# Optimization experiments

Measured on AMD Instinct MI355X. Metric: run time of the kernel, lower is better.

The kernel has to match this reference:

```python
import jax, jax.numpy as jnp
import numpy as np

B, NQ, NV, DIM, HEADS, K = 2, 2048, 2048, 256, 8, 8
HD = DIM // HEADS
HID = 4 * DIM
SCALE = HD ** -0.5
EPS = 1e-5


def setup_inputs() -> dict:
    key = jax.random.key(0)
    ks = jax.random.split(key, 40)
    r = lambda i, s: jax.random.normal(ks[i], s, jnp.float32) * 0.02
    inp = {
        'q': jax.random.normal(ks[0], (B, NQ, DIM), jnp.float32),
        'v': jax.random.normal(ks[1], (B, NV, DIM), jnp.float32),
        'q_pos': jax.random.normal(ks[2], (B, NQ, 3), jnp.float32),
        'v_pos': jax.random.normal(ks[3], (B, NV, 3), jnp.float32),
        'self_knn_index': jax.random.randint(ks[4], (B, NQ, K), 0, NQ, jnp.int32),
        'cross_knn_index': jax.random.randint(ks[5], (B, NQ, K), 0, NV, jnp.int32),
        # LayerNorms (gamma=1, beta=0)
        'norm1_g': jnp.ones(DIM), 'norm1_b': jnp.zeros(DIM),
        'normq_g': jnp.ones(DIM), 'normq_b': jnp.zeros(DIM),
        'normv_g': jnp.ones(DIM), 'normv_b': jnp.zeros(DIM),
        'norm2_g': jnp.ones(DIM), 'norm2_b': jnp.zeros(DIM),
        # self-attention (qkv_bias=False), proj has bias
        'sa_qkv_w': r(6, (DIM, 3 * DIM)),
        'sa_proj_w': r(7, (DIM, DIM)), 'sa_proj_b': jnp.zeros(DIM),
        # cross-attention: q proj and kv proj (no bias), out proj with bias
        'ca_q_w': r(8, (DIM, DIM)),
        'ca_kv_w': r(9, (DIM, 2 * DIM)),
        'ca_proj_w': r(10, (DIM, DIM)), 'ca_proj_b': jnp.zeros(DIM),
        # MLP
        'fc1_w': r(11, (DIM, HID)), 'fc1_b': jnp.zeros(HID),
        'fc2_w': r(12, (HID, DIM)), 'fc2_b': jnp.zeros(DIM),
        # kNN maps
        'knn_w': r(13, (2 * DIM, DIM)), 'knn_b': jnp.zeros(DIM),
        'merge_w': r(14, (2 * DIM, DIM)), 'merge_b': jnp.zeros(DIM),
        'knnx_w': r(15, (2 * DIM, DIM)), 'knnx_b': jnp.zeros(DIM),
        'mergex_w': r(16, (2 * DIM, DIM)), 'mergex_b': jnp.zeros(DIM),
    }
    return inp


def _ln(x, g, b):
    m = x.mean(-1, keepdims=True)
    var = x.var(-1, keepdims=True)
    return (x - m) / jnp.sqrt(var + EPS) * g + b


def _heads(x):  # [B,N,DIM] -> [B,H,N,HD]
    Bx, N, _ = x.shape
    return x.reshape(Bx, N, HEADS, HD).transpose(0, 2, 1, 3)


def _attend(qh, kh, vh, proj_w, proj_b):
    a = jax.nn.softmax(jnp.einsum('bhqd,bhkd->bhqk', qh, kh) * SCALE, axis=-1)
    o = jnp.einsum('bhqk,bhkd->bhqd', a, vh)
    Bx, _, N, _ = o.shape
    o = o.transpose(0, 2, 1, 3).reshape(Bx, N, DIM)
    return o @ proj_w + proj_b


_gather = jax.vmap(lambda pts, idx: pts[idx])  # ([N,D],[Nq,K]) -> [Nq,K,D]


def _knn_feature(qn, vn, idx):  # gather -> diff/cat -> [B,Nq,K,2D]
    local = _gather(vn, idx)                      # [B,Nq,K,D]
    qe = qn[:, :, None, :]                        # [B,Nq,1,D]
    return jnp.concatenate([local - qe, jnp.broadcast_to(qe, local.shape)], -1)


def reference(q, v, q_pos, v_pos, self_knn_index, cross_knn_index,
              norm1_g, norm1_b, normq_g, normq_b, normv_g, normv_b,
              norm2_g, norm2_b, sa_qkv_w, sa_proj_w, sa_proj_b,
              ca_q_w, ca_kv_w, ca_proj_w, ca_proj_b,
              fc1_w, fc1_b, fc2_w, fc2_b,
              knn_w, knn_b, merge_w, merge_b,
              knnx_w, knnx_b, mergex_w, mergex_b):
    # ---- self-attention block with self-kNN branch ----
    nq = _ln(q, norm1_g, norm1_b)
    qkv = nq @ sa_qkv_w
    qh, kh, vh = (_heads(t) for t in jnp.split(qkv, 3, axis=-1))
    sa_out = _attend(qh, kh, vh, sa_proj_w, sa_proj_b)
    f = _knn_feature(nq, nq, self_knn_index)
    knn_out = jax.nn.leaky_relu(f @ knn_w + knn_b, 0.2).max(axis=-2)
    q1 = jnp.concatenate([sa_out, knn_out], -1) @ merge_w + merge_b
    q = q + q1
    # ---- cross-attention block with cross-kNN branch ----
    nq2 = _ln(q, normq_g, normq_b)
    nv = _ln(v, normv_g, normv_b)
    qh = _heads(nq2 @ ca_q_w)
    kh, vh = (_heads(t) for t in jnp.split(nv @ ca_kv_w, 2, axis=-1))
    ca_out = _attend(qh, kh, vh, ca_proj_w, ca_proj_b)
    f = _knn_feature(nq2, nv, cross_knn_index)
    knnx_out = jax.nn.leaky_relu(f @ knnx_w + knnx_b, 0.2).max(axis=-2)
    q2 = jnp.concatenate([ca_out, knnx_out], -1) @ mergex_w + mergex_b
    q = q + q2
    # ---- MLP block ----
    h = _ln(q, norm2_g, norm2_b)
    h = jax.nn.gelu(h @ fc1_w + fc1_b, approximate=False)
    q = q + (h @ fc2_w + fc2_b)
    return q
```

## Files before the change

### kernel.cpp

```cpp
#include <hip/hip_runtime.h>
#include <math.h>

#define NQC   2048
#define NKVC  2048
#define DIMC  256
#define SCALEF 0.2550348810731232f

typedef short bfrag __attribute__((ext_vector_type(8)));
typedef float ffrag __attribute__((ext_vector_type(4)));
typedef unsigned short us8 __attribute__((ext_vector_type(8)));

__device__ __forceinline__ float gelu_exact(float x) {
    return 0.5f * x * (1.0f + erff(x * 0.70710678118654752f));
}
__device__ __forceinline__ unsigned short f2bf(float f) {
    union { float f; unsigned u; } v; v.f = f;
    unsigned r = v.u + 0x7FFFu + ((v.u >> 16) & 1u);
    return (unsigned short)(r >> 16);
}
__device__ __forceinline__ float bf2f(unsigned short u) {
    union { unsigned u; float f; } v; v.u = ((unsigned)u) << 16;
    return v.f;
}
__device__ __forceinline__ float fexp2(float x) {
    float r; asm("v_exp_f32 %0, %1" : "=v"(r) : "v"(x)); return r;
}
__device__ __forceinline__ unsigned cvt_pk_bf16(float lo, float hi) {
    unsigned r; asm("v_cvt_pk_bf16_f32 %0, %1, %2" : "=v"(r) : "v"(lo), "v"(hi));
    return r;
}

__device__ __forceinline__ void ln_row(
    const float* __restrict__ x, const float* __restrict__ g,
    const float* __restrict__ b, unsigned short* __restrict__ y, int row)
{
    int lane = threadIdx.x & 63;
    const float* xr = x + (size_t)row * DIMC + lane * 4;
    float4 vv = *(const float4*)xr;
    float s  = vv.x + vv.y + vv.z + vv.w;
    float sq = vv.x*vv.x + vv.y*vv.y + vv.z*vv.z + vv.w*vv.w;
    #pragma unroll
    for (int off = 32; off >= 1; off >>= 1) {
        s  += __shfl_xor(s, off);
        sq += __shfl_xor(sq, off);
    }
    float mean = s * (1.0f/DIMC);
    float inv  = rsqrtf(sq * (1.0f/DIMC) - mean*mean + 1e-5f);
    float4 gg = *(const float4*)(g + lane*4);
    float4 bb = *(const float4*)(b + lane*4);
    ushort4 o;
    o.x = f2bf((vv.x - mean) * inv * gg.x + bb.x);
    o.y = f2bf((vv.y - mean) * inv * gg.y + bb.y);
    o.z = f2bf((vv.z - mean) * inv * gg.z + bb.z);
    o.w = f2bf((vv.w - mean) * inv * gg.w + bb.w);
    *(ushort4*)(y + (size_t)row * DIMC + lane * 4) = o;
}

__global__ __launch_bounds__(256) void prep_ln(
    const float* __restrict__ qkv, const float* __restrict__ knn,
    const float* __restrict__ proj, const float* __restrict__ merge,
    const float* __restrict__ caq, const float* __restrict__ knnx,
    const float* __restrict__ cakv, const float* __restrict__ projx,
    const float* __restrict__ mergex, const float* __restrict__ fc1,
    const float* __restrict__ fc2, unsigned short* __restrict__ dst,
    const float* __restrict__ lx, const float* __restrict__ lg,
    const float* __restrict__ lb, unsigned short* __restrict__ ly,
    const float* __restrict__ vx, const float* __restrict__ vg,
    const float* __restrict__ vb, unsigned short* __restrict__ vy,
    const float* __restrict__ pb1, const float* __restrict__ mb1, float* __restrict__ bf1o,
    const float* __restrict__ pbx, const float* __restrict__ mbx, float* __restrict__ bfxo)
{
    if (blockIdx.x >= 3584) {
        const float* bp = (blockIdx.x == 3584) ? pb1 : pbx;
        const float* Wm = (blockIdx.x == 3584) ? merge : mergex;
        const float* bm = (blockIdx.x == 3584) ? mb1 : mbx;
        float* o        = (blockIdx.x == 3584) ? bf1o : bfxo;
        int m = threadIdx.x;
        float acc = bm[m];
        for (int k = 0; k < 256; ++k) acc += bp[k] * Wm[(size_t)k * 256 + m];
        o[m] = acc;
        return;
    }
    if (blockIdx.x >= 2560) {
        int row = (blockIdx.x - 2560) * 4 + (threadIdx.x >> 6);
        ln_row(vx, vg, vb, vy, row);
        return;
    }
    if (blockIdx.x >= 1536) {
        int row = (blockIdx.x - 1536) * 4 + (threadIdx.x >> 6);
        ln_row(lx, lg, lb, ly, row);
        return;
    }
    int e = (blockIdx.x * 256 + threadIdx.x) * 4;
    float v[4];
    float scale = 1.0f;
    if (e < 327680) {
        int n = e >> 8, k = e & 255;
        if (n < 768) {
            const float* s = qkv + (size_t)k * 768 + n;
            #pragma unroll
            for (int i = 0; i < 4; ++i) v[i] = s[(size_t)i * 768];
            if (n < 256) scale = SCALEF;
        } else if (n < 1024) {
            const float* s = knn + (size_t)k * 256 + (n - 768);
            #pragma unroll
            for (int i = 0; i < 4; ++i) v[i] = s[(size_t)i * 256];
        } else {
            const float* s = knn + (size_t)k * 256 + (n - 1024);
            #pragma unroll
            for (int i = 0; i < 4; ++i) v[i] = s[65536 + (size_t)i * 256] - s[(size_t)i * 256];
        }
    } else if (e < 393216) {
        int l = e - 327680;
        const float* s = proj + l;
        #pragma unroll
        for (int i = 0; i < 4; ++i) v[i] = s[i];
    } else if (e < 524288) {
        int l = e - 393216, n = l >> 9, k = l & 511;
        const float* s = merge + (size_t)k * 256 + n;
        #pragma unroll
        for (int i = 0; i < 4; ++i) v[i] = s[(size_t)i * 256];
    } else if (e < 655360) {
        int l = e - 524288, n = l >> 8, k = l & 255;
        if (n < 256) {
            const float* s = caq + (size_t)k * 256 + n;
            #pragma unroll
            for (int i = 0; i < 4; ++i) v[i] = s[(size_t)i * 256];
            scale = SCALEF;
        } else {
            const float* s = knnx + (size_t)k * 256 + (n - 256);
            #pragma unroll
            for (int i = 0; i < 4; ++i) v[i] = s[65536 + (size_t)i * 256] - s[(size_t)i * 256];
        }
    } else if (e < 851968) {
        int l = e - 655360, n = l >> 8, k = l & 255;
        if (n < 512) {
            const float* s = cakv + (size_t)k * 512 + n;
            #pragma unroll
            for (int i = 0; i < 4; ++i) v[i] = s[(size_t)i * 512];
        } else {
            const float* s = knnx + (size_t)k * 256 + (n - 512);
            #pragma unroll
            for (int i = 0; i < 4; ++i) v[i] = s[(size_t)i * 256];
        }
    } else if (e < 917504) {
        int l = e - 851968;
        const float* s = projx + l;
        #pragma unroll
        for (int i = 0; i < 4; ++i) v[i] = s[i];
    } else if (e < 1048576) {
        int l = e - 917504, n = l >> 9, k = l & 511;
        const float* s = mergex + (size_t)k * 256 + n;
        #pragma unroll
        for (int i = 0; i < 4; ++i) v[i] = s[(size_t)i * 256];
    } else if (e < 1310720) {
        int l = e - 1048576, n = l >> 8, k = l & 255;
        const float* s = fc1 + (size_t)k * 1024 + n;
        #pragma unroll
        for (int i = 0; i < 4; ++i) v[i] = s[(size_t)i * 1024];
    } else {
        int l = e - 1310720, n = l >> 10, k = l & 1023;
        const float* s = fc2 + (size_t)k * 256 + n;
        #pragma unroll
        for (int i = 0; i < 4; ++i) v[i] = s[(size_t)i * 256];
    }
    ushort4 o;
    o.x = f2bf(v[0] * scale); o.y = f2bf(v[1] * scale);
    o.z = f2bf(v[2] * scale); o.w = f2bf(v[3] * scale);
    *(ushort4*)(dst + e) = o;
}

__global__ __launch_bounds__(256) void ln_b(
    const float* __restrict__ x, const float* __restrict__ g,
    const float* __restrict__ b, unsigned short* __restrict__ y)
{
    ln_row(x, g, b, y, blockIdx.x * 4 + (threadIdx.x >> 6));
}

template<int ACT, int RESID, int OUTBF, int VTM>
__device__ __forceinline__ void gemm_body(
    const unsigned short* __restrict__ A, int lda,
    const unsigned short* __restrict__ Wt,
    const float* __restrict__ bias,
    const float* __restrict__ resid, int ldr,
    void* __restrict__ Cp, int ldc, int Kc, int row0, int col0,
    unsigned short (* __restrict__ Alds)[72],
    unsigned short (* __restrict__ Wlds)[72],
    unsigned short* __restrict__ vt, int vlo)
{
    const int tid = threadIdx.x;
    const int wid = tid >> 6, lane = tid & 63;
    const int lm = lane & 15, quad = lane >> 4;
    const int wr = wid >> 1, wc = wid & 1;
    const int ar = tid >> 2, ac = (tid & 3) * 16;
    const unsigned short* Ag = A  + (size_t)(row0 + ar) * lda + ac;
    const unsigned short* Wg = Wt + (size_t)(col0 + ar) * Kc  + ac;

    us8 a0 = *(const us8*)Ag;
    us8 a1 = *(const us8*)(Ag + 8);
    us8 w0 = *(const us8*)Wg;
    us8 w1 = *(const us8*)(Wg + 8);

    ffrag acc[2][2];
    #pragma unroll
    for (int mi = 0; mi < 2; ++mi)
        #pragma unroll
        for (int ni = 0; ni < 2; ++ni)
            acc[mi][ni] = (ffrag){0.f, 0.f, 0.f, 0.f};

    for (int k0 = 0;;) {
        __syncthreads();
        *(us8*)&Alds[ar][ac]   = a0;
        *(us8*)&Alds[ar][ac+8] = a1;
        *(us8*)&Wlds[ar][ac]   = w0;
        *(us8*)&Wlds[ar][ac+8] = w1;
        __syncthreads();
        k0 += 64;
        if (k0 < Kc) {
            a0 = *(const us8*)(Ag + k0);
            a1 = *(const us8*)(Ag + k0 + 8);
            w0 = *(const us8*)(Wg + k0);
            w1 = *(const us8*)(Wg + k0 + 8);
        }
        #pragma unroll
        for (int kc = 0; kc < 2; ++kc) {
            bfrag af[2], bw[2];
            #pragma unroll
            for (int mi = 0; mi < 2; ++mi)
                af[mi] = *(const bfrag*)&Alds[wr*32 + mi*16 + lm][kc*32 + quad*8];
            #pragma unroll
            for (int ni = 0; ni < 2; ++ni)
                bw[ni] = *(const bfrag*)&Wlds[wc*32 + ni*16 + lm][kc*32 + quad*8];
            #pragma unroll
            for (int mi = 0; mi < 2; ++mi)
                #pragma unroll
                for (int ni = 0; ni < 2; ++ni)
                    acc[mi][ni] = __builtin_amdgcn_mfma_f32_16x16x32_bf16(
                        af[mi], bw[ni], acc[mi][ni], 0, 0, 0);
        }
        if (k0 >= Kc) break;
    }
    if (VTM && col0 >= vlo && col0 - vlo < 256) {
        __syncthreads();
        #pragma unroll
        for (int mi = 0; mi < 2; ++mi) {
            #pragma unroll
            for (int ni = 0; ni < 2; ++ni) {
                int lr = wr*32 + mi*16 + quad*4;
                int lc = wc*32 + ni*16 + lm;
                #pragma unroll
                for (int r = 0; r < 4; ++r) {
                    int k = lr + r;
                    Alds[lc][((k & 15) << 2) | (k >> 4)] = f2bf(acc[mi][ni][r]);
                }
            }
        }
        __syncthreads();
        int d = tid >> 2, p0 = (tid & 3) * 16;
        int cv = col0 - vlo + d, hh = cv >> 5, dd = cv & 31;
        int bq = row0 >> 11, kblk = (row0 & 2047) >> 6;
        unsigned short* vp = vt + (((size_t)(bq * 8 + hh) * 32 + dd) * 2048)
                                + kblk * 64 + p0;
        *(us8*)vp       = *(const us8*)&Alds[d][p0];
        *(us8*)(vp + 8) = *(const us8*)&Alds[d][p0 + 8];
        return;
    }
    #pragma unroll
    for (int mi = 0; mi < 2; ++mi) {
        #pragma unroll
        for (int ni = 0; ni < 2; ++ni) {
            int gr = row0 + wr*32 + mi*16 + quad*4;
            int gc = col0 + wc*32 + ni*16 + lm;
            float bv = bias ? bias[gc] : 0.f;
            #pragma unroll
            for (int r = 0; r < 4; ++r) {
                float o = acc[mi][ni][r] + bv;
                if (ACT == 1) o = gelu_exact(o);
                if (RESID) o += resid[(size_t)(gr + r) * ldr + gc];
                if (OUTBF) ((unsigned short*)Cp)[(size_t)(gr + r) * ldc + gc] = f2bf(o);
                else       ((float*)Cp)[(size_t)(gr + r) * ldc + gc] = o;
            }
        }
    }
}

template<int ACT, int RESID, int OUTBF>
__global__ __launch_bounds__(256) void gemm64(
    const unsigned short* __restrict__ A, int lda,
    const unsigned short* __restrict__ Wt,
    const float* __restrict__ bias,
    const float* __restrict__ resid, int ldr,
    void* __restrict__ Cp, int ldc, int Kc)
{
    __shared__ unsigned short Alds[64][72];
    __shared__ unsigned short Wlds[64][72];
    gemm_body<ACT,RESID,OUTBF,0>(A, lda, Wt, bias, resid, ldr, Cp, ldc, Kc,
                                 blockIdx.y * 64, blockIdx.x * 64, Alds, Wlds,
                                 nullptr, 0);
}

__global__ __launch_bounds__(256) void gemm_qkv_fold(
    const unsigned short* __restrict__ XB, const unsigned short* __restrict__ WT1,
    unsigned short* __restrict__ A1,
    const unsigned short* __restrict__ WTmerge, const unsigned short* __restrict__ projbf,
    unsigned short* __restrict__ WTf1,
    const unsigned short* __restrict__ WTmergex, const unsigned short* __restrict__ projxbf,
    unsigned short* __restrict__ WTfx,
    unsigned short* __restrict__ VT)
{
    __shared__ unsigned short Alds[64][72];
    __shared__ unsigned short Wlds[64][72];
    const unsigned short *A, *Wt; unsigned short* C;
    int lda, ldc, row0, col0, vlo;
    if (blockIdx.y >= 64) {
        if (blockIdx.x >= 16) return;
        row0 = (blockIdx.x >> 2) * 64; col0 = (blockIdx.x & 3) * 64;
        lda = 512; ldc = 256; vlo = 1 << 30;
        if (blockIdx.y == 64) { A = WTmerge;  Wt = projbf;  C = WTf1; }
        else                  { A = WTmergex; Wt = projxbf; C = WTfx; }
    } else {
        A = XB; Wt = WT1; C = A1; lda = 256; ldc = 1280; vlo = 512;
        row0 = blockIdx.y * 64; col0 = blockIdx.x * 64;
    }
    gemm_body<0,0,1,1>(A, lda, Wt, nullptr, nullptr, 0, C, ldc, 256, row0, col0,
                       Alds, Wlds, VT, vlo);
}

template<int ACT, int RESID, int OUTBF>
__global__ __launch_bounds__(512) void gemm64x8(
    const unsigned short* __restrict__ A, int lda,
    const unsigned short* __restrict__ Wt,
    const float* __restrict__ bias,
    const float* __restrict__ resid, int ldr,
    void* __restrict__ Cp, int ldc, int Kc)
{
    __shared__ unsigned short Alds[2][64][72];
    __shared__ unsigned short Wlds[2][64][72];
    __shared__ float Red[64][68];
    const int tid = threadIdx.x;
    const int g = tid >> 8;
    const int t = tid & 255;
    const int wid2 = (tid >> 6) & 3, lane = tid & 63;
    const int lm = lane & 15, quad = lane >> 4;
    const int wr = wid2 >> 1, wc = wid2 & 1;
    const int row0 = blockIdx.y * 64, col0 = blockIdx.x * 64;
    const int ar = t >> 2, ac = (t & 3) * 16;
    const int KH = Kc >> 1;
    const unsigned short* Ag = A  + (size_t)(row0 + ar) * lda + g * KH + ac;
    const unsigned short* Wg = Wt + (size_t)(col0 + ar) * Kc  + g * KH + ac;

    us8 a0 = *(const us8*)Ag;
    us8 a1 = *(const us8*)(Ag + 8);
    us8 w0 = *(const us8*)Wg;
    us8 w1 = *(const us8*)(Wg + 8);

    ffrag acc[2][2];
    #pragma unroll
    for (int mi = 0; mi < 2; ++mi)
        #pragma unroll
        for (int ni = 0; ni < 2; ++ni)
            acc[mi][ni] = (ffrag){0.f, 0.f, 0.f, 0.f};

    for (int k0 = 0;;) {
        __syncthreads();
        *(us8*)&Alds[g][ar][ac]   = a0;
        *(us8*)&Alds[g][ar][ac+8] = a1;
        *(us8*)&Wlds[g][ar][ac]   = w0;
        *(us8*)&Wlds[g][ar][ac+8] = w1;
        __syncthreads();
        k0 += 64;
        if (k0 < KH) {
            a0 = *(const us8*)(Ag + k0);
            a1 = *(const us8*)(Ag + k0 + 8);
            w0 = *(const us8*)(Wg + k0);
            w1 = *(const us8*)(Wg + k0 + 8);
        }
        #pragma unroll
        for (int kc = 0; kc < 2; ++kc) {
            bfrag af[2], bw[2];
            #pragma unroll
            for (int mi = 0; mi < 2; ++mi)
                af[mi] = *(const bfrag*)&Alds[g][wr*32 + mi*16 + lm][kc*32 + quad*8];
            #pragma unroll
            for (int ni = 0; ni < 2; ++ni)
                bw[ni] = *(const bfrag*)&Wlds[g][wc*32 + ni*16 + lm][kc*32 + quad*8];
            #pragma unroll
            for (int mi = 0; mi < 2; ++mi)
                #pragma unroll
                for (int ni = 0; ni < 2; ++ni)
                    acc[mi][ni] = __builtin_amdgcn_mfma_f32_16x16x32_bf16(
                        af[mi], bw[ni], acc[mi][ni], 0, 0, 0);
        }
        if (k0 >= KH) break;
    }
    __syncthreads();
    if (g == 1) {
        #pragma unroll
        for (int mi = 0; mi < 2; ++mi)
            #pragma unroll
            for (int ni = 0; ni < 2; ++ni) {
                int lr = wr*32 + mi*16 + quad*4;
                int lc = wc*32 + ni*16 + lm;
                #pragma unroll
                for (int r = 0; r < 4; ++r)
                    Red[lr + r][lc] = acc[mi][ni][r];
            }
    }
    __syncthreads();
    if (g == 0) {
        #pragma unroll
        for (int mi = 0; mi < 2; ++mi) {
            #pragma unroll
            for (int ni = 0; ni < 2; ++ni) {
                int lr = wr*32 + mi*16 + quad*4;
                int lc = wc*32 + ni*16 + lm;
                int gr = row0 + lr;
                int gc = col0 + lc;
                float bv = bias ? bias[gc] : 0.f;
                #pragma unroll
                for (int r = 0; r < 4; ++r) {
                    float o = acc[mi][ni][r] + Red[lr + r][lc] + bv;
                    if (ACT == 1) o = gelu_exact(o);
                    if (RESID) o += resid[(size_t)(gr + r) * ldr + gc];
                    if (OUTBF) ((unsigned short*)Cp)[(size_t)(gr + r) * ldc + gc] = f2bf(o);
                    else       ((float*)Cp)[(size_t)(gr + r) * ldc + gc] = o;
                }
            }
        }
    }
}

__global__ __launch_bounds__(512) void gemm64x8f(
    const unsigned short* __restrict__ O,
    const unsigned short* __restrict__ Akn,
    const unsigned short* __restrict__ W0,
    const unsigned short* __restrict__ W1,
    const float* __restrict__ bias,
    const float* __restrict__ resid,
    float* __restrict__ Cp)
{
    __shared__ unsigned short Alds[2][64][72];
    __shared__ unsigned short Wlds[2][64][72];
    __shared__ float Red[64][68];
    const int tid = threadIdx.x;
    const int g = tid >> 8;
    const int t = tid & 255;
    const int wid2 = (tid >> 6) & 3, lane = tid & 63;
    const int lm = lane & 15, quad = lane >> 4;
    const int wr = wid2 >> 1, wc = wid2 & 1;
    const int row0 = blockIdx.y * 64, col0 = blockIdx.x * 64;
    const int ar = t >> 2, ac = (t & 3) * 16;
    const int grow = row0 + ar;

    const unsigned short* Ag = g ? Akn + (size_t)grow * 512 + ac
                                 : O   + (size_t)grow * 256 + ac;
    const unsigned short* Wg = g ? W1 + (size_t)(col0 + ar) * 512 + ac
                                 : W0 + (size_t)(col0 + ar) * 256 + ac;

    us8 a0 = *(const us8*)Ag;
    us8 a1 = *(const us8*)(Ag + 8);
    us8 w0 = *(const us8*)Wg;
    us8 w1 = *(const us8*)(Wg + 8);

    ffrag acc[2][2];
    #pragma unroll
    for (int mi = 0; mi < 2; ++mi)
        #pragma unroll
        for (int ni = 0; ni < 2; ++ni)
            acc[mi][ni] = (ffrag){0.f, 0.f, 0.f, 0.f};

    for (int k0 = 0;;) {
        __syncthreads();
        *(us8*)&Alds[g][ar][ac]   = a0;
        *(us8*)&Alds[g][ar][ac+8] = a1;
        *(us8*)&Wlds[g][ar][ac]   = w0;
        *(us8*)&Wlds[g][ar][ac+8] = w1;
        __syncthreads();
        k0 += 64;
        if (k0 < 256) {
            a0 = *(const us8*)(Ag + k0);
            a1 = *(const us8*)(Ag + k0 + 8);
            w0 = *(const us8*)(Wg + k0);
            w1 = *(const us8*)(Wg + k0 + 8);
        }
        #pragma unroll
        for (int kc = 0; kc < 2; ++kc) {
            bfrag af[2], bw[2];
            #pragma unroll
            for (int mi = 0; mi < 2; ++mi)
                af[mi] = *(const bfrag*)&Alds[g][wr*32 + mi*16 + lm][kc*32 + quad*8];
            #pragma unroll
            for (int ni = 0; ni < 2; ++ni)
                bw[ni] = *(const bfrag*)&Wlds[g][wc*32 + ni*16 + lm][kc*32 + quad*8];
            #pragma unroll
            for (int mi = 0; mi < 2; ++mi)
                #pragma unroll
                for (int ni = 0; ni < 2; ++ni)
                    acc[mi][ni] = __builtin_amdgcn_mfma_f32_16x16x32_bf16(
                        af[mi], bw[ni], acc[mi][ni], 0, 0, 0);
        }
        if (k0 >= 256) break;
    }
    __syncthreads();
    if (g == 1) {
        #pragma unroll
        for (int mi = 0; mi < 2; ++mi)
            #pragma unroll
            for (int ni = 0; ni < 2; ++ni) {
                int lr = wr*32 + mi*16 + quad*4;
                int lc = wc*32 + ni*16 + lm;
                #pragma unroll
                for (int r = 0; r < 4; ++r)
                    Red[lr + r][lc] = acc[mi][ni][r];
            }
    }
    __syncthreads();
    if (g == 0) {
        #pragma unroll
        for (int mi = 0; mi < 2; ++mi) {
            #pragma unroll
            for (int ni = 0; ni < 2; ++ni) {
                int lr = wr*32 + mi*16 + quad*4;
                int lc = wc*32 + ni*16 + lm;
                int gr = row0 + lr;
                int gc = col0 + lc;
                float bv = bias[gc];
                #pragma unroll
                for (int r = 0; r < 4; ++r)
                    Cp[(size_t)(gr + r) * 256 + gc] =
                        acc[mi][ni][r] + Red[lr + r][lc] + bv
                        + resid[(size_t)(gr + r) * 256 + gc];
            }
        }
    }
}

__global__ __launch_bounds__(256) void gemm64_dual(
    const unsigned short* __restrict__ XB,
    const unsigned short* __restrict__ NVB,
    const unsigned short* __restrict__ WT2,
    const unsigned short* __restrict__ WT3,
    unsigned short* __restrict__ A2,
    unsigned short* __restrict__ A3,
    unsigned short* __restrict__ VT)
{
    __shared__ unsigned short Alds[64][72];
    __shared__ unsigned short Wlds[64][72];
    const unsigned short* A; const unsigned short* Wt;
    unsigned short* C; int ldc, col0, vlo;
    if (blockIdx.x < 8) { A = XB;  Wt = WT2; C = A2; ldc = 512; col0 = blockIdx.x * 64; vlo = 1 << 30; }
    else                { A = NVB; Wt = WT3; C = A3; ldc = 768; col0 = (blockIdx.x - 8) * 64; vlo = 256; }
    gemm_body<0,0,1,1>(A, 256, Wt, nullptr, nullptr, 0, C, ldc, 256,
                       blockIdx.y * 64, col0, Alds, Wlds, VT, vlo);
}

__global__ __launch_bounds__(256) void attn_gather(
    const unsigned short* __restrict__ Qp, int ldq,
    const unsigned short* __restrict__ Kp, int ldk,
    const unsigned short* __restrict__ VT,
    unsigned short* __restrict__ Op,
    const unsigned short* __restrict__ P, int ldp,
    const unsigned short* __restrict__ Base, int ldb,
    const float* __restrict__ gbias, const int* __restrict__ idx,
    unsigned short* __restrict__ gout, int ldgo)
{
    __shared__ unsigned short Klds[64][40];
    __shared__ __align__(16) unsigned short Vt[32][72];
    __shared__ __align__(16) unsigned short Plds[4][16][72];
    int tid = threadIdx.x, wid = tid >> 6, lane = tid & 63;

    if (blockIdx.z >= 1) {
        int gbid = blockIdx.x + 64 * (blockIdx.y + 8 * (blockIdx.z - 1));
        int q = gbid * 4 + wid;
        int b = q >> 11;
        int c = lane * 4;
        ushort4 bu = *(const ushort4*)(Base + (size_t)q * ldb + c);
        float4 bi = *(const float4*)(gbias + c);
        float bsx = bf2f(bu.x) + bi.x, bsy = bf2f(bu.y) + bi.y;
        float bsz = bf2f(bu.z) + bi.z, bsw = bf2f(bu.w) + bi.w;
        float4 acc = make_float4(-3e38f, -3e38f, -3e38f, -3e38f);
        const int* ip = idx + (size_t)q * 8;
        #pragma unroll
        for (int k = 0; k < 8; ++k) {
            int j = ip[k];
            ushort4 pu = *(const ushort4*)(P + ((size_t)(b * NKVC + j)) * ldp + c);
            float t;
            t = bsx + bf2f(pu.x); t = t > 0.f ? t : 0.2f * t; acc.x = fmaxf(acc.x, t);
            t = bsy + bf2f(pu.y); t = t > 0.f ? t : 0.2f * t; acc.y = fmaxf(acc.y, t);
            t = bsz + bf2f(pu.z); t = t > 0.f ? t : 0.2f * t; acc.z = fmaxf(acc.z, t);
            t = bsw + bf2f(pu.w); t = t > 0.f ? t : 0.2f * t; acc.w = fmaxf(acc.w, t);
        }
        ushort4 o;
        o.x = f2bf(acc.x); o.y = f2bf(acc.y); o.z = f2bf(acc.z); o.w = f2bf(acc.w);
        *(ushort4*)(gout + (size_t)q * ldgo + c) = o;
        return;
    }

    int bb = blockIdx.x >> 5, qc = blockIdx.x & 31;
    int h = blockIdx.y;
    int hoff = h * 32;
    int lm = lane & 15, quad = lane >> 4;
    size_t qbase  = (size_t)bb * NQC;
    size_t kvbase = (size_t)bb * NKVC;
    int q0 = qc * 64 + wid * 16;

    bfrag aq = *(const bfrag*)(Qp + (qbase + q0 + lm) * (size_t)ldq + hoff + quad * 8);

    float l_r[4] = {0.f, 0.f, 0.f, 0.f};
    ffrag oacc[2];
    oacc[0] = (ffrag){0.f, 0.f, 0.f, 0.f};
    oacc[1] = (ffrag){0.f, 0.f, 0.f, 0.f};

    const int kkey = tid >> 2, kd0 = (tid & 3) * 8;
    const int vrow = tid >> 3, vp0 = (tid & 7) * 8;
    const unsigned short* kg0 = Kp + (kvbase + kkey) * (size_t)ldk + hoff + kd0;
    const unsigned short* vg0 = VT + (((size_t)bb * 8 + h) * 32 + vrow) * 2048 + vp0;

    for (int kt = 0; kt < 32; ++kt) {
        us8 kv = *(const us8*)(kg0 + (size_t)kt * 64 * ldk);
        us8 vv = *(const us8*)(vg0 + kt * 64);
        __syncthreads();
        *(us8*)&Klds[kkey][kd0] = kv;
        *(us8*)&Vt[vrow][vp0]   = vv;
        __syncthreads();

        ffrag sacc[4];
        #pragma unroll
        for (int t = 0; t < 4; ++t) {
            bfrag bk = *(const bfrag*)&Klds[t*16 + lm][quad * 8];
            sacc[t] = __builtin_amdgcn_mfma_f32_16x16x32_bf16(
                aq, bk, (ffrag){0.f,0.f,0.f,0.f}, 0, 0, 0);
        }

        #pragma unroll
        for (int r = 0; r < 4; ++r) {
            float p0 = fexp2(sacc[0][r]), p1 = fexp2(sacc[1][r]);
            float p2 = fexp2(sacc[2][r]), p3 = fexp2(sacc[3][r]);
            l_r[r] += (p0 + p1) + (p2 + p3);
            *(uint2*)&Plds[wid][quad*4 + r][lm << 2] =
                make_uint2(cvt_pk_bf16(p0, p1), cvt_pk_bf16(p2, p3));
        }
        asm volatile("s_waitcnt lgkmcnt(0)" ::: "memory");

        #pragma unroll
        for (int kc = 0; kc < 2; ++kc) {
            bfrag ap  = *(const bfrag*)&Plds[wid][lm][kc*32 + quad*8];
            bfrag bv0 = *(const bfrag*)&Vt[lm][kc*32 + quad*8];
            bfrag bv1 = *(const bfrag*)&Vt[16 + lm][kc*32 + quad*8];
            oacc[0] = __builtin_amdgcn_mfma_f32_16x16x32_bf16(ap, bv0, oacc[0], 0, 0, 0);
            oacc[1] = __builtin_amdgcn_mfma_f32_16x16x32_bf16(ap, bv1, oacc[1], 0, 0, 0);
        }
    }
    #pragma unroll
    for (int r = 0; r < 4; ++r) {
        float a = l_r[r];
        a += __shfl_xor(a, 1); a += __shfl_xor(a, 2);
        a += __shfl_xor(a, 4); a += __shfl_xor(a, 8);
        l_r[r] = 1.0f / a;
    }
    #pragma unroll
    for (int nt = 0; nt < 2; ++nt)
        #pragma unroll
        for (int r = 0; r < 4; ++r)
            Op[(qbase + q0 + quad*4 + r) * 256 + hoff + nt*16 + lm]
                = f2bf(oacc[nt][r] * l_r[r]);
}

extern "C" void kernel_launch(void* const* d_in, const int* in_sizes, int n_in,
                              void* d_out, int out_size, void* d_ws, size_t ws_size,
                              hipStream_t stream) {
    const float* q_in   = (const float*)d_in[0];
    const float* v_in   = (const float*)d_in[1];
    const int*   idx_s  = (const int*)d_in[4];
    const int*   idx_x  = (const int*)d_in[5];
    const float* n1g = (const float*)d_in[6],  *n1b = (const float*)d_in[7];
    const float* nqg = (const float*)d_in[8],  *nqb = (const float*)d_in[9];
    const float* nvg = (const float*)d_in[10], *nvb = (const float*)d_in[11];
    const float* n2g = (const float*)d_in[12], *n2b = (const float*)d_in[13];
    const float* sa_qkv_w  = (const float*)d_in[14];
    const float* sa_proj_w = (const float*)d_in[15];
    const float* sa_proj_b = (const float*)d_in[16];
    const float* ca_q_w    = (const float*)d_in[17];
    const float* ca_kv_w   = (const float*)d_in[18];
    const float* ca_proj_w = (const float*)d_in[19];
    const float* ca_proj_b = (const float*)d_in[20];
    const float* fc1_w = (const float*)d_in[21], *fc1_b = (const float*)d_in[22];
    const float* fc2_w = (const float*)d_in[23], *fc2_b = (const float*)d_in[24];
    const float* knn_w   = (const float*)d_in[25], *knn_b   = (const float*)d_in[26];
    const float* merge_w = (const float*)d_in[27], *merge_b = (const float*)d_in[28];
    const float* knnx_w  = (const float*)d_in[29], *knnx_b  = (const float*)d_in[30];
    const float* mergex_w = (const float*)d_in[31], *mergex_b = (const float*)d_in[32];
    float* out = (float*)d_out;

    unsigned short* A1      = (unsigned short*)d_ws;
    unsigned short* A2      = A1;
    unsigned short* A3      = A1 + (size_t)4096 * 512;
    unsigned short* Hb      = A1;
    unsigned short* KN      = A1 + (size_t)4096 * 1280;
    unsigned short* CC      = KN;
    unsigned short* XB      = CC + (size_t)4096 * 512;
    unsigned short* NVB     = XB + (size_t)4096 * 256;
    unsigned short* WT      = NVB + (size_t)4096 * 256;
    unsigned short* WT1     = WT;
    unsigned short* projbf  = WT + 327680;
    unsigned short* WTmerge = WT + 393216;
    unsigned short* WT2     = WT + 524288;
    unsigned short* WT3     = WT + 655360;
    unsigned short* projxbf = WT + 851968;
    unsigned short* WTmergex= WT + 917504;
    unsigned short* WTfc1   = WT + 1048576;
    unsigned short* WTfc2   = WT + 1310720;
    unsigned short* Opart   = WT + 1572864;
    unsigned short* WTf1    = Opart + (size_t)4096 * 256;
    unsigned short* WTfx    = WTf1 + 65536;
    float* bf1 = (float*)(WTfx + 65536);
    float* bfx = bf1 + 256;
    unsigned short* VT = (unsigned short*)(bfx + 256);

    dim3 blk(256), blk8(512);
    dim3 gAG(64, 8, 3);

    prep_ln<<<dim3(3586), blk, 0, stream>>>(sa_qkv_w, knn_w, sa_proj_w, merge_w,
        ca_q_w, knnx_w, ca_kv_w, ca_proj_w, mergex_w, fc1_w, fc2_w, WT,
        q_in, n1g, n1b, XB,
        v_in, nvg, nvb, NVB,
        sa_proj_b, merge_b, bf1,
        ca_proj_b, mergex_b, bfx);

    gemm_qkv_fold<<<dim3(20,66), blk, 0, stream>>>(XB, WT1, A1,
        WTmerge, projbf, WTf1, WTmergex, projxbf, WTfx, VT);
    attn_gather<<<gAG, blk, 0, stream>>>(A1, 1280, A1+256, 1280, VT,
        Opart, A1+768, 1280, A1+1024, 1280, knn_b, idx_s, CC+256, 512);
    gemm64x8f<<<dim3(4,64), blk8, 0, stream>>>(Opart, CC+256,
        WTf1, WTmerge+256, bf1, q_in, out);

    ln_b<<<dim3(1024), blk, 0, stream>>>(out, nqg, nqb, XB);
    gemm64_dual<<<dim3(20,64), blk, 0, stream>>>(XB, NVB, WT2, WT3, A2, A3, VT);
    attn_gather<<<gAG, blk, 0, stream>>>(A2, 512, A3, 768, VT,
        Opart, A3+512, 768, A2+256, 512, knnx_b, idx_x, CC+256, 512);
    gemm64x8f<<<dim3(4,64), blk8, 0, stream>>>(Opart, CC+256,
        WTfx, WTmergex+256, bfx, out, out);

    ln_b<<<dim3(1024), blk, 0, stream>>>(out, n2g, n2b, XB);
    gemm64<1,0,1><<<dim3(16,64), blk, 0, stream>>>(XB, 256, WTfc1,
        fc1_b, nullptr, 0, Hb, 1024, 256);
    gemm64x8<0,1,0><<<dim3(4,64), blk8, 0, stream>>>(Hb, 1024, WTfc2,
        fc2_b, out, 256, out, 256, 1024);
}
```

Baseline: 248.3 us.

## Fuse LayerNorm into GEMM A-tile loads and tile weight transposes via LDS

Drops the separate LayerNorm kernels (ln_b launches and the norm1 part of prep). Each GEMM block now computes row mean and variance from fp32 activations and normalizes to bf16 while loading its A tiles. This removes two launches and the bf16 round trip through global memory. In exchange, every column block recomputes the row statistics and rereads fp32 rows. The weight prep kernel also now transposes 64x64 tiles through shared memory with vectorized coalesced loads and stores, replacing strided scalar reads.

```diff
diff --git a/kernel.cpp b/kernel.cpp
--- a/kernel.cpp
+++ b/kernel.cpp
@@ -56,130 +56,149 @@
     *(ushort4*)(y + (size_t)row * DIMC + lane * 4) = o;
 }
 
-__global__ __launch_bounds__(256) void prep_ln(
+__device__ __forceinline__ void ln_frag(
+    const float* __restrict__ xr, const float* __restrict__ lng,
+    const float* __restrict__ lnb, int cc, float mean, float inv,
+    us8& o0, us8& o1)
+{
+    float4 x0 = *(const float4*)(xr + cc);
+    float4 x1 = *(const float4*)(xr + cc + 4);
+    float4 x2 = *(const float4*)(xr + cc + 8);
+    float4 x3 = *(const float4*)(xr + cc + 12);
+    float4 g0 = *(const float4*)(lng + cc);
+    float4 g1 = *(const float4*)(lng + cc + 4);
+    float4 g2 = *(const float4*)(lng + cc + 8);
+    float4 g3 = *(const float4*)(lng + cc + 12);
+    float4 b0 = *(const float4*)(lnb + cc);
+    float4 b1 = *(const float4*)(lnb + cc + 4);
+    float4 b2 = *(const float4*)(lnb + cc + 8);
+    float4 b3 = *(const float4*)(lnb + cc + 12);
+    union { us8 v; unsigned short s[8]; } u0, u1;
+    u0.s[0] = f2bf(((x0.x - mean) * inv) * g0.x + b0.x);
+    u0.s[1] = f2bf(((x0.y - mean) * inv) * g0.y + b0.y);
+    u0.s[2] = f2bf(((x0.z - mean) * inv) * g0.z + b0.z);
+    u0.s[3] = f2bf(((x0.w - mean) * inv) * g0.w + b0.w);
+    u0.s[4] = f2bf(((x1.x - mean) * inv) * g1.x + b1.x);
+    u0.s[5] = f2bf(((x1.y - mean) * inv) * g1.y + b1.y);
+    u0.s[6] = f2bf(((x1.z - mean) * inv) * g1.z + b1.z);
+    u0.s[7] = f2bf(((x1.w - mean) * inv) * g1.w + b1.w);
+    u1.s[0] = f2bf(((x2.x - mean) * inv) * g2.x + b2.x);
+    u1.s[1] = f2bf(((x2.y - mean) * inv) * g2.y + b2.y);
+    u1.s[2] = f2bf(((x2.z - mean) * inv) * g2.z + b2.z);
+    u1.s[3] = f2bf(((x2.w - mean) * inv) * g2.w + b2.w);
+    u1.s[4] = f2bf(((x3.x - mean) * inv) * g3.x + b3.x);
+    u1.s[5] = f2bf(((x3.y - mean) * inv) * g3.y + b3.y);
+    u1.s[6] = f2bf(((x3.z - mean) * inv) * g3.z + b3.z);
+    u1.s[7] = f2bf(((x3.w - mean) * inv) * g3.w + b3.w);
+    o0 = u0.v; o1 = u1.v;
+}
+
+__global__ __launch_bounds__(256) void prep_w(
     const float* __restrict__ qkv, const float* __restrict__ knn,
     const float* __restrict__ proj, const float* __restrict__ merge,
     const float* __restrict__ caq, const float* __restrict__ knnx,
     const float* __restrict__ cakv, const float* __restrict__ projx,
     const float* __restrict__ mergex, const float* __restrict__ fc1,
     const float* __restrict__ fc2, unsigned short* __restrict__ dst,
-    const float* __restrict__ lx, const float* __restrict__ lg,
-    const float* __restrict__ lb, unsigned short* __restrict__ ly,
     const float* __restrict__ vx, const float* __restrict__ vg,
     const float* __restrict__ vb, unsigned short* __restrict__ vy,
     const float* __restrict__ pb1, const float* __restrict__ mb1, float* __restrict__ bf1o,
     const float* __restrict__ pbx, const float* __restrict__ mbx, float* __restrict__ bfxo)
 {
-    if (blockIdx.x >= 3584) {
-        const float* bp = (blockIdx.x == 3584) ? pb1 : pbx;
-        const float* Wm = (blockIdx.x == 3584) ? merge : mergex;
-        const float* bm = (blockIdx.x == 3584) ? mb1 : mbx;
-        float* o        = (blockIdx.x == 3584) ? bf1o : bfxo;
-        int m = threadIdx.x;
+    __shared__ unsigned short T[64][72];
+    int blk = blockIdx.x, tid = threadIdx.x;
+    if (blk >= 1504) {
+        const float* bp = (blk == 1504) ? pb1 : pbx;
+        const float* Wm = (blk == 1504) ? merge : mergex;
+        const float* bm = (blk == 1504) ? mb1 : mbx;
+        float* o        = (blk == 1504) ? bf1o : bfxo;
+        int m = tid;
         float acc = bm[m];
         for (int k = 0; k < 256; ++k) acc += bp[k] * Wm[(size_t)k * 256 + m];
         o[m] = acc;
         return;
     }
-    if (blockIdx.x >= 2560) {
-        int row = (blockIdx.x - 2560) * 4 + (threadIdx.x >> 6);
-        ln_row(vx, vg, vb, vy, row);
+    if (blk >= 480) {
+        ln_row(vx, vg, vb, vy, (blk - 480) * 4 + (tid >> 6));
         return;
     }
-    if (blockIdx.x >= 1536) {
-        int row = (blockIdx.x - 1536) * 4 + (threadIdx.x >> 6);
-        ln_row(lx, lg, lb, ly, row);
+    if (blk >= 352) {
+        int l = blk - 352;
+        const float* s; unsigned short* d;
+        if (l < 64) { s = proj;  d = dst + 327680; }
+        else        { s = projx; d = dst + 851968; l -= 64; }
+        int e = (l * 256 + tid) * 4;
+        float4 v = *(const float4*)(s + e);
+        ushort4 o;
+        o.x = f2bf(v.x); o.y = f2bf(v.y); o.z = f2bf(v.z); o.w = f2bf(v.w);
+        *(ushort4*)(d + e) = o;
         return;
     }
-    int e = (blockIdx.x * 256 + threadIdx.x) * 4;
-    float v[4];
-    float scale = 1.0f;
-    if (e < 327680) {
-        int n = e >> 8, k = e & 255;
-        if (n < 768) {
-            const float* s = qkv + (size_t)k * 768 + n;
-            #pragma unroll
-            for (int i = 0; i < 4; ++i) v[i] = s[(size_t)i * 768];
-            if (n < 256) scale = SCALEF;
-        } else if (n < 1024) {
-            const float* s = knn + (size_t)k * 256 + (n - 768);
-            #pragma unroll
-            for (int i = 0; i < 4; ++i) v[i] = s[(size_t)i * 256];
-        } else {
-            const float* s = knn + (size_t)k * 256 + (n - 1024);
-            #pragma unroll
-            for (int i = 0; i < 4; ++i) v[i] = s[65536 + (size_t)i * 256] - s[(size_t)i * 256];
-        }
-    } else if (e < 393216) {
-        int l = e - 327680;
-        const float* s = proj + l;
-        #pragma unroll
-        for (int i = 0; i < 4; ++i) v[i] = s[i];
-    } else if (e < 524288) {
-        int l = e - 393216, n = l >> 9, k = l & 511;
-        const float* s = merge + (size_t)k * 256 + n;
-        #pragma unroll
-        for (int i = 0; i < 4; ++i) v[i] = s[(size_t)i * 256];
-    } else if (e < 655360) {
-        int l = e - 524288, n = l >> 8, k = l & 255;
-        if (n < 256) {
-            const float* s = caq + (size_t)k * 256 + n;
-            #pragma unroll
-            for (int i = 0; i < 4; ++i) v[i] = s[(size_t)i * 256];
-            scale = SCALEF;
-        } else {
-            const float* s = knnx + (size_t)k * 256 + (n - 256);
-            #pragma unroll
-            for (int i = 0; i < 4; ++i) v[i] = s[65536 + (size_t)i * 256] - s[(size_t)i * 256];
-        }
-    } else if (e < 851968) {
-        int l = e - 655360, n = l >> 8, k = l & 255;
-        if (n < 512) {
-            const float* s = cakv + (size_t)k * 512 + n;
-            #pragma unroll
-            for (int i = 0; i < 4; ++i) v[i] = s[(size_t)i * 512];
-        } else {
-            const float* s = knnx + (size_t)k * 256 + (n - 512);
-            #pragma unroll
-            for (int i = 0; i < 4; ++i) v[i] = s[(size_t)i * 256];
-        }
-    } else if (e < 917504) {
-        int l = e - 851968;
-        const float* s = projx + l;
-        #pragma unroll
-        for (int i = 0; i < 4; ++i) v[i] = s[i];
-    } else if (e < 1048576) {
-        int l = e - 917504, n = l >> 9, k = l & 511;
-        const float* s = mergex + (size_t)k * 256 + n;
-        #pragma unroll
-        for (int i = 0; i < 4; ++i) v[i] = s[(size_t)i * 256];
-    } else if (e < 1310720) {
-        int l = e - 1048576, n = l >> 8, k = l & 255;
-        const float* s = fc1 + (size_t)k * 1024 + n;
-        #pragma unroll
-        for (int i = 0; i < 4; ++i) v[i] = s[(size_t)i * 1024];
-    } else {
-        int l = e - 1310720, n = l >> 10, k = l & 1023;
-        const float* s = fc2 + (size_t)k * 256 + n;
-        #pragma unroll
-        for (int i = 0; i < 4; ++i) v[i] = s[(size_t)i * 256];
-    }
-    ushort4 o;
-    o.x = f2bf(v[0] * scale); o.y = f2bf(v[1] * scale);
-    o.z = f2bf(v[2] * scale); o.w = f2bf(v[3] * scale);
-    *(ushort4*)(dst + e) = o;
-}
-
-__global__ __launch_bounds__(256) void ln_b(
-    const float* __restrict__ x, const float* __restrict__ g,
-    const float* __restrict__ b, unsigned short* __restrict__ y)
-{
-    ln_row(x, g, b, y, blockIdx.x * 4 + (threadIdx.x >> 6));
-}
-
-template<int ACT, int RESID, int OUTBF, int VTM>
+    int t = blk;
+    const float* src; const float* src2 = nullptr; int sN;
+    unsigned short* dp; int dK; float scale = 1.0f; int n0, k0;
+    if (t < 48)       { src = qkv;          sN = 768;  dp = dst;           dK = 256;
+                        n0 = (t % 12) * 64; k0 = (t / 12) * 64; if (n0 < 256) scale = SCALEF; }
+    else if (t < 64)  { int u = t - 48;  src = knn;          sN = 256; dp = dst + 196608; dK = 256;
+                        n0 = (u & 3) * 64; k0 = (u >> 2) * 64; }
+    else if (t < 80)  { int u = t - 64;  src = knn + 65536;  src2 = knn; sN = 256; dp = dst + 262144; dK = 256;
+                        n0 = (u & 3) * 64; k0 = (u >> 2) * 64; }
+    else if (t < 112) { int u = t - 80;  src = merge;        sN = 256; dp = dst + 393216; dK = 512;
+                        n0 = (u & 3) * 64; k0 = (u >> 2) * 64; }
+    else if (t < 128) { int u = t - 112; src = caq;          sN = 256; dp = dst + 524288; dK = 256;
+                        n0 = (u & 3) * 64; k0 = (u >> 2) * 64; scale = SCALEF; }
+    else if (t < 144) { int u = t - 128; src = knnx + 65536; src2 = knnx; sN = 256; dp = dst + 589824; dK = 256;
+                        n0 = (u & 3) * 64; k0 = (u >> 2) * 64; }
+    else if (t < 176) { int u = t - 144; src = cakv;         sN = 512; dp = dst + 655360; dK = 256;
+                        n0 = (u & 7) * 64; k0 = (u >> 3) * 64; }
+    else if (t < 192) { int u = t - 176; src = knnx;         sN = 256; dp = dst + 786432; dK = 256;
+                        n0 = (u & 3) * 64; k0 = (u >> 2) * 64; }
+    else if (t < 224) { int u = t - 192; src = mergex;       sN = 256; dp = dst + 917504; dK = 512;
+                        n0 = (u & 3) * 64; k0 = (u >> 2) * 64; }
+    else if (t < 288) { int u = t - 224; src = fc1;          sN = 1024; dp = dst + 1048576; dK = 256;
+                        n0 = (u & 15) * 64; k0 = (u >> 4) * 64; }
+    else              { int u = t - 288; src = fc2;          sN = 256; dp = dst + 1310720; dK = 1024;
+                        n0 = (u & 3) * 64; k0 = (u >> 2) * 64; }
+    int r = tid >> 2, c0 = (tid & 3) * 16;
+    float va[16];
+    {
+        const float* sp = src + (size_t)(k0 + r) * sN + n0 + c0;
+        float4 f0 = *(const float4*)(sp);
+        float4 f1 = *(const float4*)(sp + 4);
+        float4 f2 = *(const float4*)(sp + 8);
+        float4 f3 = *(const float4*)(sp + 12);
+        va[0]=f0.x; va[1]=f0.y; va[2]=f0.z;  va[3]=f0.w;
+        va[4]=f1.x; va[5]=f1.y; va[6]=f1.z;  va[7]=f1.w;
+        va[8]=f2.x; va[9]=f2.y; va[10]=f2.z; va[11]=f2.w;
+        va[12]=f3.x; va[13]=f3.y; va[14]=f3.z; va[15]=f3.w;
+        if (src2) {
+            const float* s2 = src2 + (size_t)(k0 + r) * sN + n0 + c0;
+            float4 h0 = *(const float4*)(s2);
+            float4 h1 = *(const float4*)(s2 + 4);
+            float4 h2 = *(const float4*)(s2 + 8);
+            float4 h3 = *(const float4*)(s2 + 12);
+            va[0]-=h0.x; va[1]-=h0.y; va[2]-=h0.z;  va[3]-=h0.w;
+            va[4]-=h1.x; va[5]-=h1.y; va[6]-=h1.z;  va[7]-=h1.w;
+            va[8]-=h2.x; va[9]-=h2.y; va[10]-=h2.z; va[11]-=h2.w;
+            va[12]-=h3.x; va[13]-=h3.y; va[14]-=h3.z; va[15]-=h3.w;
+        }
+    }
+    #pragma unroll
+    for (int i = 0; i < 16; ++i) T[c0 + i][r] = f2bf(va[i] * scale);
+    __syncthreads();
+    {
+        int n = tid >> 2, kk = (tid & 3) * 16;
+        unsigned short* d = dp + (size_t)(n0 + n) * dK + k0 + kk;
+        *(us8*)d       = *(const us8*)&T[n][kk];
+        *(us8*)(d + 8) = *(const us8*)&T[n][kk + 8];
+    }
+}
+
+template<int ACT, int RESID, int OUTBF, int VTM, int LNA>
 __device__ __forceinline__ void gemm_body(
     const unsigned short* __restrict__ A, int lda,
+    const float* __restrict__ Af, const float* __restrict__ lng,
+    const float* __restrict__ lnb,
     const unsigned short* __restrict__ Wt,
     const float* __restrict__ bias,
     const float* __restrict__ resid, int ldr,
@@ -193,13 +212,31 @@
     const int lm = lane & 15, quad = lane >> 4;
     const int wr = wid >> 1, wc = wid & 1;
     const int ar = tid >> 2, ac = (tid & 3) * 16;
-    const unsigned short* Ag = A  + (size_t)(row0 + ar) * lda + ac;
-    const unsigned short* Wg = Wt + (size_t)(col0 + ar) * Kc  + ac;
-
-    us8 a0 = *(const us8*)Ag;
-    us8 a1 = *(const us8*)(Ag + 8);
-    us8 w0 = *(const us8*)Wg;
-    us8 w1 = *(const us8*)(Wg + 8);
+    float mean = 0.f, inv = 0.f;
+    const float* xr = nullptr;
+    if (LNA) {
+        xr = Af + (size_t)(row0 + ar) * 256;
+        float s = 0.f, sq = 0.f;
+        int cb = (tid & 3) * 64;
+        #pragma unroll
+        for (int i = 0; i < 16; ++i) {
+            float4 v = *(const float4*)(xr + cb + i * 4);
+            s  += (v.x + v.y) + (v.z + v.w);
+            sq += (v.x*v.x + v.y*v.y) + (v.z*v.z + v.w*v.w);
+        }
+        s  += __shfl_xor(s, 1);  s  += __shfl_xor(s, 2);
+        sq += __shfl_xor(sq, 1); sq += __shfl_xor(sq, 2);
+        mean = s * (1.0f/256.0f);
+        inv  = rsqrtf(sq * (1.0f/256.0f) - mean*mean + 1e-5f);
+    }
+    const unsigned short* Ag = LNA ? nullptr : A + (size_t)(row0 + ar) * lda + ac;
+    const unsigned short* Wg = Wt + (size_t)(col0 + ar) * Kc + ac;
+
+    us8 a0, a1, w0, w1;
+    if (LNA) ln_frag(xr, lng, lnb, ac, mean, inv, a0, a1);
+    else { a0 = *(const us8*)Ag; a1 = *(const us8*)(Ag + 8); }
+    w0 = *(const us8*)Wg;
+    w1 = *(const us8*)(Wg + 8);
 
     ffrag acc[2][2];
     #pragma unroll
@@ -217,8 +254,8 @@
         __syncthreads();
         k0 += 64;
         if (k0 < Kc) {
-            a0 = *(const us8*)(Ag + k0);
-            a1 = *(const us8*)(Ag + k0 + 8);
+            if (LNA) ln_frag(xr, lng, lnb, k0 + ac, mean, inv, a0, a1);
+            else { a0 = *(const us8*)(Ag + k0); a1 = *(const us8*)(Ag + k0 + 8); }
             w0 = *(const us8*)(Wg + k0);
             w1 = *(const us8*)(Wg + k0 + 8);
         }
@@ -284,24 +321,10 @@
     }
 }
 
-template<int ACT, int RESID, int OUTBF>
-__global__ __launch_bounds__(256) void gemm64(
-    const unsigned short* __restrict__ A, int lda,
-    const unsigned short* __restrict__ Wt,
-    const float* __restrict__ bias,
-    const float* __restrict__ resid, int ldr,
-    void* __restrict__ Cp, int ldc, int Kc)
-{
-    __shared__ unsigned short Alds[64][72];
-    __shared__ unsigned short Wlds[64][72];
-    gemm_body<ACT,RESID,OUTBF,0>(A, lda, Wt, bias, resid, ldr, Cp, ldc, Kc,
-                                 blockIdx.y * 64, blockIdx.x * 64, Alds, Wlds,
-                                 nullptr, 0);
-}
-
 __global__ __launch_bounds__(256) void gemm_qkv_fold(
-    const unsigned short* __restrict__ XB, const unsigned short* __restrict__ WT1,
-    unsigned short* __restrict__ A1,
+    const float* __restrict__ qin, const float* __restrict__ n1g,
+    const float* __restrict__ n1b,
+    const unsigned short* __restrict__ WT1, unsigned short* __restrict__ A1,
     const unsigned short* __restrict__ WTmerge, const unsigned short* __restrict__ projbf,
     unsigned short* __restrict__ WTf1,
     const unsigned short* __restrict__ WTmergex, const unsigned short* __restrict__ projxbf,
@@ -310,20 +333,56 @@
 {
     __shared__ unsigned short Alds[64][72];
     __shared__ unsigned short Wlds[64][72];
-    const unsigned short *A, *Wt; unsigned short* C;
-    int lda, ldc, row0, col0, vlo;
     if (blockIdx.y >= 64) {
         if (blockIdx.x >= 16) return;
-        row0 = (blockIdx.x >> 2) * 64; col0 = (blockIdx.x & 3) * 64;
-        lda = 512; ldc = 256; vlo = 1 << 30;
-        if (blockIdx.y == 64) { A = WTmerge;  Wt = projbf;  C = WTf1; }
-        else                  { A = WTmergex; Wt = projxbf; C = WTfx; }
+        int row0 = (blockIdx.x >> 2) * 64, col0 = (blockIdx.x & 3) * 64;
+        if (blockIdx.y == 64)
+            gemm_body<0,0,1,0,0>(WTmerge, 512, nullptr, nullptr, nullptr, projbf,
+                nullptr, nullptr, 0, WTf1, 256, 256, row0, col0, Alds, Wlds, nullptr, 0);
+        else
+            gemm_body<0,0,1,0,0>(WTmergex, 512, nullptr, nullptr, nullptr, projxbf,
+                nullptr, nullptr, 0, WTfx, 256, 256, row0, col0, Alds, Wlds, nullptr, 0);
     } else {
-        A = XB; Wt = WT1; C = A1; lda = 256; ldc = 1280; vlo = 512;
-        row0 = blockIdx.y * 64; col0 = blockIdx.x * 64;
-    }
-    gemm_body<0,0,1,1>(A, lda, Wt, nullptr, nullptr, 0, C, ldc, 256, row0, col0,
-                       Alds, Wlds, VT, vlo);
+        gemm_body<0,0,1,1,1>(nullptr, 0, qin, n1g, n1b, WT1,
+            nullptr, nullptr, 0, A1, 1280, 256, blockIdx.y * 64, blockIdx.x * 64,
+            Alds, Wlds, VT, 512);
+    }
+}
+
+__global__ __launch_bounds__(256) void gemm64_dual(
+    const float* __restrict__ outp, const float* __restrict__ nqg,
+    const float* __restrict__ nqb,
+    const unsigned short* __restrict__ NVB,
+    const unsigned short* __restrict__ WT2,
+    const unsigned short* __restrict__ WT3,
+    unsigned short* __restrict__ A2,
+    unsigned short* __restrict__ A3,
+    unsigned short* __restrict__ VT)
+{
+    __shared__ unsigned short Alds[64][72];
+    __shared__ unsigned short Wlds[64][72];
+    if (blockIdx.x < 8)
+        gemm_body<0,0,1,0,1>(nullptr, 0, outp, nqg, nqb, WT2,
+            nullptr, nullptr, 0, A2, 512, 256, blockIdx.y * 64, blockIdx.x * 64,
+            Alds, Wlds, nullptr, 0);
+    else
+        gemm_body<0,0,1,1,0>(NVB, 256, nullptr, nullptr, nullptr, WT3,
+            nullptr, nullptr, 0, A3, 768, 256, blockIdx.y * 64, (blockIdx.x - 8) * 64,
+            Alds, Wlds, VT, 256);
+}
+
+__global__ __launch_bounds__(256) void gemm64_ln(
+    const float* __restrict__ Af, const float* __restrict__ lng,
+    const float* __restrict__ lnb,
+    const unsigned short* __restrict__ Wt,
+    const float* __restrict__ bias,
+    unsigned short* __restrict__ Cp, int ldc)
+{
+    __shared__ unsigned short Alds[64][72];
+    __shared__ unsigned short Wlds[64][72];
+    gemm_body<1,0,1,0,1>(nullptr, 0, Af, lng, lnb, Wt, bias, nullptr, 0,
+                         Cp, ldc, 256, blockIdx.y * 64, blockIdx.x * 64,
+                         Alds, Wlds, nullptr, 0);
 }
 
 template<int ACT, int RESID, int OUTBF>
@@ -533,25 +592,6 @@
             }
         }
     }
-}
-
-__global__ __launch_bounds__(256) void gemm64_dual(
-    const unsigned short* __restrict__ XB,
-    const unsigned short* __restrict__ NVB,
-    const unsigned short* __restrict__ WT2,
-    const unsigned short* __restrict__ WT3,
-    unsigned short* __restrict__ A2,
-    unsigned short* __restrict__ A3,
-    unsigned short* __restrict__ VT)
-{
-    __shared__ unsigned short Alds[64][72];
-    __shared__ unsigned short Wlds[64][72];
-    const unsigned short* A; const unsigned short* Wt;
-    unsigned short* C; int ldc, col0, vlo;
-    if (blockIdx.x < 8) { A = XB;  Wt = WT2; C = A2; ldc = 512; col0 = blockIdx.x * 64; vlo = 1 << 30; }
-    else                { A = NVB; Wt = WT3; C = A3; ldc = 768; col0 = (blockIdx.x - 8) * 64; vlo = 256; }
-    gemm_body<0,0,1,1>(A, 256, Wt, nullptr, nullptr, 0, C, ldc, 256,
-                       blockIdx.y * 64, col0, Alds, Wlds, VT, vlo);
 }
 
 __global__ __launch_bounds__(256) void attn_gather(
@@ -720,30 +760,28 @@
     dim3 blk(256), blk8(512);
     dim3 gAG(64, 8, 3);
 
-    prep_ln<<<dim3(3586), blk, 0, stream>>>(sa_qkv_w, knn_w, sa_proj_w, merge_w,
+    prep_w<<<dim3(1506), blk, 0, stream>>>(sa_qkv_w, knn_w, sa_proj_w, merge_w,
         ca_q_w, knnx_w, ca_kv_w, ca_proj_w, mergex_w, fc1_w, fc2_w, WT,
-        q_in, n1g, n1b, XB,
         v_in, nvg, nvb, NVB,
         sa_proj_b, merge_b, bf1,
         ca_proj_b, mergex_b, bfx);
 
-    gemm_qkv_fold<<<dim3(20,66), blk, 0, stream>>>(XB, WT1, A1,
+    gemm_qkv_fold<<<dim3(20,66), blk, 0, stream>>>(q_in, n1g, n1b, WT1, A1,
         WTmerge, projbf, WTf1, WTmergex, projxbf, WTfx, VT);
     attn_gather<<<gAG, blk, 0, stream>>>(A1, 1280, A1+256, 1280, VT,
         Opart, A1+768, 1280, A1+1024, 1280, knn_b, idx_s, CC+256, 512);
     gemm64x8f<<<dim3(4,64), blk8, 0, stream>>>(Opart, CC+256,
         WTf1, WTmerge+256, bf1, q_in, out);
 
-    ln_b<<<dim3(1024), blk, 0, stream>>>(out, nqg, nqb, XB);
-    gemm64_dual<<<dim3(20,64), blk, 0, stream>>>(XB, NVB, WT2, WT3, A2, A3, VT);
+    gemm64_dual<<<dim3(20,64), blk, 0, stream>>>(out, nqg, nqb, NVB,
+        WT2, WT3, A2, A3, VT);
     attn_gather<<<gAG, blk, 0, stream>>>(A2, 512, A3, 768, VT,
         Opart, A3+512, 768, A2+256, 512, knnx_b, idx_x, CC+256, 512);
     gemm64x8f<<<dim3(4,64), blk8, 0, stream>>>(Opart, CC+256,
         WTfx, WTmergex+256, bfx, out, out);
 
-    ln_b<<<dim3(1024), blk, 0, stream>>>(out, n2g, n2b, XB);
-    gemm64<1,0,1><<<dim3(16,64), blk, 0, stream>>>(XB, 256, WTfc1,
-        fc1_b, nullptr, 0, Hb, 1024, 256);
+    gemm64_ln<<<dim3(16,64), blk, 0, stream>>>(out, n2g, n2b, WTfc1,
+        fc1_b, Hb, 1024);
     gemm64x8<0,1,0><<<dim3(4,64), blk8, 0, stream>>>(Hb, 1024, WTfc2,
         fc2_b, out, 256, out, 256, 1024);
 }
```

Result: slower. 287.4 us (+15.8%).
